# Kernel optimization log

Measured on AMD Instinct MI355X. Metric: run time of the kernel, lower is better.

Reference implementation:

```python
import jax, jax.numpy as jnp
import numpy as np

C_LEN, Q_LEN, B, H = 2048, 512, 32, 256


def setup_inputs() -> dict:
    key = jax.random.key(0)
    k1, k2 = jax.random.split(key)
    content_vec = jax.random.normal(k1, (C_LEN, B, H), dtype=jnp.float32)
    question_vec = jax.random.normal(k2, (Q_LEN, B, H), dtype=jnp.float32)
    question_mask = jnp.ones((B, Q_LEN), dtype=jnp.int32)
    return {"content_vec": content_vec, "question_vec": question_vec, "question_mask": question_mask}


def reference(content_vec, question_vec, question_mask):
    # scores: (B, c_len, q_len) = content (b,c,h) @ question^T (b,h,q)
    scores = jnp.einsum('cbh,qbh->bcq', content_vec, question_vec)
    # additive -inf mask where question_mask == 0, broadcast over c_len
    neg_inf = jnp.asarray(-jnp.inf, dtype=scores.dtype)
    scores = jnp.where(question_mask[:, None, :] == 0, neg_inf, scores)
    attn = jax.nn.softmax(scores, axis=-1)  # (B, c_len, q_len)
    # weighted sum of question vectors -> back to (c_len, B, H)
    out = jnp.einsum('bcq,qbh->cbh', attn, question_vec)
    return out
```

## Files before the change

kernel.cpp:

```cpp
#include <hip/hip_runtime.h>

#define C_LENX 2048
#define Q_LENX 512
#define BATCH  32
#define HDIM   256
#define BH     8192
#define CBLK   64
#define QBLK   32
#define NQT    16
#define NWAVES 4
#define TILE_BYTES 32768
#define OFF_QT 16384

typedef __attribute__((ext_vector_type(8))) _Float16 f16x8;
typedef __attribute__((ext_vector_type(4))) float f32x4;

__device__ __forceinline__ unsigned short f2h_bits(float x) {
    union { _Float16 h; unsigned short u; } cv;
    cv.h = (_Float16)x;
    return cv.u;
}
__device__ __forceinline__ float h2f_bits(unsigned short u) {
    union { unsigned short u; _Float16 h; } cv;
    cv.u = u;
    return (float)cv.h;
}

__device__ __forceinline__ void stage16(const void* gsrc, void* ldst) {
    __builtin_amdgcn_global_load_lds(
        (const __attribute__((address_space(1))) unsigned int*)gsrc,
        (__attribute__((address_space(3))) unsigned int*)ldst, 16, 0, 0);
}

__global__ __launch_bounds__(256)
void q_prep(const float* __restrict__ question, unsigned char* __restrict__ blob)
{
    __shared__ unsigned short sHf[QBLK][264];
    const int tid = threadIdx.x;
    const int b  = blockIdx.x >> 4;
    const int t  = blockIdx.x & 15;
    const float* qbase = question + (size_t)(t * QBLK) * BH + b * HDIM;
    unsigned char* tb = blob + (size_t)(b * NQT + t) * TILE_BYTES;

    #pragma unroll
    for (int i = 0; i < 8; ++i) {
        int e  = tid + i * 256;
        int qr = e >> 6;
        int h4 = (e & 63) << 2;
        float4 x = *reinterpret_cast<const float4*>(qbase + (size_t)qr * BH + h4);
        ushort4 hv;
        hv.x = f2h_bits(x.x); hv.y = f2h_bits(x.y);
        hv.z = f2h_bits(x.z); hv.w = f2h_bits(x.w);
        *reinterpret_cast<ushort4*>(&sHf[qr][h4]) = hv;
        int c = h4 >> 3;
        *reinterpret_cast<ushort4*>(tb + qr * 512 + ((c ^ (qr & 7)) << 4) + ((h4 & 7) << 1)) = hv;
    }
    __syncthreads();
    #pragma unroll
    for (int i = 0; i < 8; ++i) {
        int e  = tid + i * 256;
        int h  = e >> 3;
        int q4 = (e & 7) << 2;
        ushort4 v;
        v.x = sHf[q4 + 0][h]; v.y = sHf[q4 + 1][h];
        v.z = sHf[q4 + 2][h]; v.w = sHf[q4 + 3][h];
        int m  = h * 4 + (q4 >> 3);
        int ms = m ^ ((m >> 3) & 7);
        *reinterpret_cast<ushort4*>(tb + OFF_QT + (ms << 4) + ((q4 & 4) << 1)) = v;
    }
}

__global__ __launch_bounds__(256, 2)
void s2s_attn(const float* __restrict__ content,
              const unsigned char* __restrict__ blob,
              const int*   __restrict__ qmask,
              float*       __restrict__ out)
{
    __shared__ __attribute__((aligned(16))) unsigned char sBuf[2 * TILE_BYTES];

    const int tid  = threadIdx.x;
    const int wid  = tid >> 6;
    const int lane = tid & 63;
    const int lr   = lane & 15;
    const int lg   = lane >> 4;

    const int lin = (blockIdx.x & 7) * 128 + (blockIdx.x >> 3);
    const int ct = lin & 31;
    const int b  = lin >> 5;
    const int c0 = ct * CBLK;

    {
        const unsigned char* tb0 = blob + (size_t)(b * NQT) * TILE_BYTES;
        #pragma unroll
        for (int j = 0; j < 8; ++j) {
            int seg = wid * 8 + j;
            stage16(tb0 + seg * 1024 + lane * 16, sBuf + seg * 1024);
        }
    }

    f16x8 chi[8];
    {
        const float* cbase = content + (size_t)(c0 + wid*16 + lr) * BH + b*HDIM + lg*8;
        #pragma unroll
        for (int kc = 0; kc < 8; ++kc) {
            float4 x0 = *reinterpret_cast<const float4*>(cbase + kc*32);
            float4 x1 = *reinterpret_cast<const float4*>(cbase + kc*32 + 4);
            float xs[8] = {x0.x,x0.y,x0.z,x0.w,x1.x,x1.y,x1.z,x1.w};
            #pragma unroll
            for (int j = 0; j < 8; ++j)
                chi[kc][j] = (_Float16)xs[j];
        }
    }

    f32x4 acc[16];
    #pragma unroll
    for (int n = 0; n < 16; ++n) { f32x4 z = {0.f,0.f,0.f,0.f}; acc[n] = z; }
    float m_run = -INFINITY;
    float l_run = 0.f;

    __syncthreads();

    for (int t = 0; t < NQT; ++t) {
        const unsigned char* qf = sBuf + (t & 1) * TILE_BYTES;
        const unsigned char* qt = qf + OFF_QT;

        if (t + 1 < NQT) {
            const unsigned char* tbn = blob + (size_t)(b * NQT + t + 1) * TILE_BYTES;
            unsigned char* db = sBuf + ((t + 1) & 1) * TILE_BYTES;
            #pragma unroll
            for (int j = 0; j < 8; ++j) {
                int seg = wid * 8 + j;
                stage16(tbn + seg * 1024 + lane * 16, db + seg * 1024);
            }
        }
        const unsigned mw = (unsigned)__ballot(qmask[b * Q_LENX + t * QBLK + (lane & 31)] != 0);

        f32x4 zz = {0.f,0.f,0.f,0.f};
        f32x4 s0a=zz, s0b=zz, s1a=zz, s1b=zz;
        const unsigned swz = (unsigned)(lr & 7);
        __builtin_amdgcn_s_setprio(1);
        #pragma unroll
        for (int kc = 0; kc < 8; kc += 2) {
            unsigned offA = (unsigned)((kc*4 + lg) ^ swz) << 4;
            unsigned offB = (unsigned)(((kc+1)*4 + lg) ^ swz) << 4;
            f16x8 qa0 = *reinterpret_cast<const f16x8*>(qf + lr*512 + offA);
            f16x8 qa1 = *reinterpret_cast<const f16x8*>(qf + (16+lr)*512 + offA);
            f16x8 qb0 = *reinterpret_cast<const f16x8*>(qf + lr*512 + offB);
            f16x8 qb1 = *reinterpret_cast<const f16x8*>(qf + (16+lr)*512 + offB);
            s0a = __builtin_amdgcn_mfma_f32_16x16x32_f16(qa0, chi[kc],   s0a, 0, 0, 0);
            s1a = __builtin_amdgcn_mfma_f32_16x16x32_f16(qa1, chi[kc],   s1a, 0, 0, 0);
            s0b = __builtin_amdgcn_mfma_f32_16x16x32_f16(qb0, chi[kc+1], s0b, 0, 0, 0);
            s1b = __builtin_amdgcn_mfma_f32_16x16x32_f16(qb1, chi[kc+1], s1b, 0, 0, 0);
        }
        __builtin_amdgcn_s_setprio(0);
        f32x4 sacc0 = s0a + s0b;
        f32x4 sacc1 = s1a + s1b;

        f16x8 vf[16];
        #pragma unroll
        for (int n = 0; n < 16; ++n) {
            int h = n*16 + lr;
            int m = h*4 + lg;
            int ms = m ^ ((m >> 3) & 7);
            vf[n] = *reinterpret_cast<const f16x8*>(qt + (ms << 4));
        }

        float p[8];
        float tmax = -INFINITY;
        #pragma unroll
        for (int r = 0; r < 4; ++r) {
            float v0 = ((mw >> (lg*4 + r))      & 1u) ? sacc0[r] : -INFINITY;
            float v1 = ((mw >> (16 + lg*4 + r)) & 1u) ? sacc1[r] : -INFINITY;
            p[r] = v0; p[4 + r] = v1;
            tmax = fmaxf(tmax, fmaxf(v0, v1));
        }
        tmax = fmaxf(tmax, __shfl_xor(tmax, 16, 64));
        tmax = fmaxf(tmax, __shfl_xor(tmax, 32, 64));

        if (__ballot(tmax > m_run + 4.0f)) {
            float mnew = fmaxf(m_run, tmax);
            float scale = 1.f;
            if (mnew != -INFINITY) { scale = __expf(m_run - mnew); m_run = mnew; }
            l_run *= scale;
            float sc0 = __shfl(scale, lg*4 + 0, 16);
            float sc1 = __shfl(scale, lg*4 + 1, 16);
            float sc2 = __shfl(scale, lg*4 + 2, 16);
            float sc3 = __shfl(scale, lg*4 + 3, 16);
            #pragma unroll
            for (int n = 0; n < 16; ++n) {
                acc[n][0] *= sc0; acc[n][1] *= sc1;
                acc[n][2] *= sc2; acc[n][3] *= sc3;
            }
        }

        unsigned short pb[8];
        float psum = 0.f;
        if (m_run == -INFINITY) {
            #pragma unroll
            for (int i = 0; i < 8; ++i) pb[i] = 0;
        } else {
            #pragma unroll
            for (int i = 0; i < 8; ++i) {
                float e = __expf(p[i] - m_run);
                pb[i] = f2h_bits(e);
                psum += h2f_bits(pb[i]);
            }
        }
        psum += __shfl_xor(psum, 16, 64);
        psum += __shfl_xor(psum, 32, 64);
        l_run += psum;

        unsigned d0 = (unsigned)pb[0] | ((unsigned)pb[1] << 16);
        unsigned d1 = (unsigned)pb[2] | ((unsigned)pb[3] << 16);
        unsigned d2 = (unsigned)pb[4] | ((unsigned)pb[5] << 16);
        unsigned d3 = (unsigned)pb[6] | ((unsigned)pb[7] << 16);
        int srcA = ((2*lg) & 3) * 16 + lr;
        int srcB = srcA + 16;
        bool hi = (lg >= 2);
        unsigned a0 = (unsigned)__shfl((int)d0, srcA, 64);
        unsigned a1 = (unsigned)__shfl((int)d1, srcA, 64);
        unsigned a2 = (unsigned)__shfl((int)d2, srcA, 64);
        unsigned a3 = (unsigned)__shfl((int)d3, srcA, 64);
        unsigned b0 = (unsigned)__shfl((int)d0, srcB, 64);
        unsigned b1 = (unsigned)__shfl((int)d1, srcB, 64);
        unsigned b2 = (unsigned)__shfl((int)d2, srcB, 64);
        unsigned b3 = (unsigned)__shfl((int)d3, srcB, 64);
        union { unsigned u[4]; f16x8 v; } pu;
        pu.u[0] = hi ? a2 : a0;
        pu.u[1] = hi ? a3 : a1;
        pu.u[2] = hi ? b2 : b0;
        pu.u[3] = hi ? b3 : b1;
        f16x8 pfrag = pu.v;

        __builtin_amdgcn_s_setprio(1);
        #pragma unroll
        for (int n = 0; n < 16; ++n)
            acc[n] = __builtin_amdgcn_mfma_f32_16x16x32_f16(pfrag, vf[n], acc[n], 0, 0, 0);
        __builtin_amdgcn_s_setprio(0);

        __syncthreads();
    }

    float linv = 1.f / l_run;
    float rinv[4];
    rinv[0] = __shfl(linv, lg*4 + 0, 16);
    rinv[1] = __shfl(linv, lg*4 + 1, 16);
    rinv[2] = __shfl(linv, lg*4 + 2, 16);
    rinv[3] = __shfl(linv, lg*4 + 3, 16);
    float* obase = out + (size_t)(c0 + wid*16) * BH + b*HDIM;
    #pragma unroll
    for (int n = 0; n < 16; ++n) {
        #pragma unroll
        for (int r = 0; r < 4; ++r)
            obase[(size_t)(lg*4 + r) * BH + n*16 + lr] = acc[n][r] * rinv[r];
    }
}

extern "C" void kernel_launch(void* const* d_in, const int* in_sizes, int n_in,
                              void* d_out, int out_size, void* d_ws, size_t ws_size,
                              hipStream_t stream) {
    const float* content  = (const float*)d_in[0];
    const float* question = (const float*)d_in[1];
    const int*   mask     = (const int*)d_in[2];
    float*       out      = (float*)d_out;

    unsigned char* blob = (unsigned char*)d_ws;

    q_prep<<<BATCH * NQT, 256, 0, stream>>>(question, blob);
    s2s_attn<<<C_LENX / CBLK * BATCH, 256, 0, stream>>>(content, blob, mask, out);
}
```

Before: 88.90 us.

## Compute transposed PV product so probabilities feed MFMA without cross-lane shuffles

The PV matmul is reformulated as out^T = V^T * P^T using two 16x16x16 MFMAs per output tile. The softmax probabilities now sit directly in the B-operand layout, which removes the eight cross-lane shuffles and the rescale broadcasts. The V^T tile layout written by q_prep is changed to match and no longer uses the swizzle. Output accumulators now hold a row per lane, so stores become 16-byte vector writes. The cost is twice as many, smaller MFMA instructions, and the unswizzled LDS reads may hit bank conflicts.

Result: slower. 92.09 us (+3.6%).

```diff
diff --git a/kernel.cpp b/kernel.cpp
--- a/kernel.cpp
+++ b/kernel.cpp
@@ -13,17 +13,13 @@
 #define OFF_QT 16384
 
 typedef __attribute__((ext_vector_type(8))) _Float16 f16x8;
+typedef __attribute__((ext_vector_type(4))) _Float16 f16x4;
 typedef __attribute__((ext_vector_type(4))) float f32x4;
 
 __device__ __forceinline__ unsigned short f2h_bits(float x) {
     union { _Float16 h; unsigned short u; } cv;
     cv.h = (_Float16)x;
     return cv.u;
-}
-__device__ __forceinline__ float h2f_bits(unsigned short u) {
-    union { unsigned short u; _Float16 h; } cv;
-    cv.u = u;
-    return (float)cv.h;
 }
 
 __device__ __forceinline__ void stage16(const void* gsrc, void* ldst) {
@@ -57,16 +53,20 @@
     }
     __syncthreads();
     #pragma unroll
-    for (int i = 0; i < 8; ++i) {
-        int e  = tid + i * 256;
-        int h  = e >> 3;
-        int q4 = (e & 7) << 2;
-        ushort4 v;
-        v.x = sHf[q4 + 0][h]; v.y = sHf[q4 + 1][h];
-        v.z = sHf[q4 + 2][h]; v.w = sHf[q4 + 3][h];
-        int m  = h * 4 + (q4 >> 3);
-        int ms = m ^ ((m >> 3) & 7);
-        *reinterpret_cast<ushort4*>(tb + OFF_QT + (ms << 4) + ((q4 & 4) << 1)) = v;
+    for (int i = 0; i < 4; ++i) {
+        int c   = tid + i * 256;
+        int n   = c >> 6;
+        int hr  = (c >> 2) & 15;
+        int lg4 = c & 3;
+        int h  = n * 16 + hr;
+        int q0 = lg4 * 4;
+        ushort4 lo, hi;
+        lo.x = sHf[q0 + 0][h]; lo.y = sHf[q0 + 1][h];
+        lo.z = sHf[q0 + 2][h]; lo.w = sHf[q0 + 3][h];
+        hi.x = sHf[16 + q0 + 0][h]; hi.y = sHf[16 + q0 + 1][h];
+        hi.z = sHf[16 + q0 + 2][h]; hi.w = sHf[16 + q0 + 3][h];
+        *reinterpret_cast<ushort4*>(tb + OFF_QT + c * 16)     = lo;
+        *reinterpret_cast<ushort4*>(tb + OFF_QT + c * 16 + 8) = hi;
     }
 }
 
@@ -156,14 +156,10 @@
         f32x4 sacc0 = s0a + s0b;
         f32x4 sacc1 = s1a + s1b;
 
-        f16x8 vf[16];
-        #pragma unroll
-        for (int n = 0; n < 16; ++n) {
-            int h = n*16 + lr;
-            int m = h*4 + lg;
-            int ms = m ^ ((m >> 3) & 7);
-            vf[n] = *reinterpret_cast<const f16x8*>(qt + (ms << 4));
-        }
+        f16x8 vt[16];
+        #pragma unroll
+        for (int n = 0; n < 16; ++n)
+            vt[n] = *reinterpret_cast<const f16x8*>(qt + (((n*16 + lr)*4 + lg) << 4));
 
         float p[8];
         float tmax = -INFINITY;
@@ -182,77 +178,49 @@
             float scale = 1.f;
             if (mnew != -INFINITY) { scale = __expf(m_run - mnew); m_run = mnew; }
             l_run *= scale;
-            float sc0 = __shfl(scale, lg*4 + 0, 16);
-            float sc1 = __shfl(scale, lg*4 + 1, 16);
-            float sc2 = __shfl(scale, lg*4 + 2, 16);
-            float sc3 = __shfl(scale, lg*4 + 3, 16);
-            #pragma unroll
-            for (int n = 0; n < 16; ++n) {
-                acc[n][0] *= sc0; acc[n][1] *= sc1;
-                acc[n][2] *= sc2; acc[n][3] *= sc3;
-            }
-        }
-
-        unsigned short pb[8];
+            #pragma unroll
+            for (int n = 0; n < 16; ++n)
+                acc[n] *= scale;
+        }
+
+        _Float16 ph[8];
         float psum = 0.f;
         if (m_run == -INFINITY) {
             #pragma unroll
-            for (int i = 0; i < 8; ++i) pb[i] = 0;
+            for (int i = 0; i < 8; ++i) ph[i] = (_Float16)0.f;
         } else {
             #pragma unroll
             for (int i = 0; i < 8; ++i) {
                 float e = __expf(p[i] - m_run);
-                pb[i] = f2h_bits(e);
-                psum += h2f_bits(pb[i]);
+                ph[i] = (_Float16)e;
+                psum += (float)ph[i];
             }
         }
         psum += __shfl_xor(psum, 16, 64);
         psum += __shfl_xor(psum, 32, 64);
         l_run += psum;
 
-        unsigned d0 = (unsigned)pb[0] | ((unsigned)pb[1] << 16);
-        unsigned d1 = (unsigned)pb[2] | ((unsigned)pb[3] << 16);
-        unsigned d2 = (unsigned)pb[4] | ((unsigned)pb[5] << 16);
-        unsigned d3 = (unsigned)pb[6] | ((unsigned)pb[7] << 16);
-        int srcA = ((2*lg) & 3) * 16 + lr;
-        int srcB = srcA + 16;
-        bool hi = (lg >= 2);
-        unsigned a0 = (unsigned)__shfl((int)d0, srcA, 64);
-        unsigned a1 = (unsigned)__shfl((int)d1, srcA, 64);
-        unsigned a2 = (unsigned)__shfl((int)d2, srcA, 64);
-        unsigned a3 = (unsigned)__shfl((int)d3, srcA, 64);
-        unsigned b0 = (unsigned)__shfl((int)d0, srcB, 64);
-        unsigned b1 = (unsigned)__shfl((int)d1, srcB, 64);
-        unsigned b2 = (unsigned)__shfl((int)d2, srcB, 64);
-        unsigned b3 = (unsigned)__shfl((int)d3, srcB, 64);
-        union { unsigned u[4]; f16x8 v; } pu;
-        pu.u[0] = hi ? a2 : a0;
-        pu.u[1] = hi ? a3 : a1;
-        pu.u[2] = hi ? b2 : b0;
-        pu.u[3] = hi ? b3 : b1;
-        f16x8 pfrag = pu.v;
-
+        f16x4 bp0 = {ph[0], ph[1], ph[2], ph[3]};
+        f16x4 bp1 = {ph[4], ph[5], ph[6], ph[7]};
         __builtin_amdgcn_s_setprio(1);
         #pragma unroll
-        for (int n = 0; n < 16; ++n)
-            acc[n] = __builtin_amdgcn_mfma_f32_16x16x32_f16(pfrag, vf[n], acc[n], 0, 0, 0);
+        for (int n = 0; n < 16; ++n) {
+            f16x4 alo = {vt[n][0], vt[n][1], vt[n][2], vt[n][3]};
+            f16x4 ahi = {vt[n][4], vt[n][5], vt[n][6], vt[n][7]};
+            acc[n] = __builtin_amdgcn_mfma_f32_16x16x16f16(alo, bp0, acc[n], 0, 0, 0);
+            acc[n] = __builtin_amdgcn_mfma_f32_16x16x16f16(ahi, bp1, acc[n], 0, 0, 0);
+        }
         __builtin_amdgcn_s_setprio(0);
 
         __syncthreads();
     }
 
-    float linv = 1.f / l_run;
-    float rinv[4];
-    rinv[0] = __shfl(linv, lg*4 + 0, 16);
-    rinv[1] = __shfl(linv, lg*4 + 1, 16);
-    rinv[2] = __shfl(linv, lg*4 + 2, 16);
-    rinv[3] = __shfl(linv, lg*4 + 3, 16);
-    float* obase = out + (size_t)(c0 + wid*16) * BH + b*HDIM;
+    float rinv = 1.f / l_run;
+    float* orow = out + (size_t)(c0 + wid*16 + lr) * BH + b*HDIM;
     #pragma unroll
     for (int n = 0; n < 16; ++n) {
-        #pragma unroll
-        for (int r = 0; r < 4; ++r)
-            obase[(size_t)(lg*4 + r) * BH + n*16 + lr] = acc[n][r] * rinv[r];
+        f32x4 v = acc[n] * rinv;
+        *reinterpret_cast<f32x4*>(orow + n*16 + lg*4) = v;
     }
 }
 
```
